# Kernel optimization log

Measured on AMD Instinct MI355X. Metric: run time of the kernel, lower is better.

## Reference

```python
import jax, jax.numpy as jnp
import numpy as np


def _bilinear_sample(image, flow):
    # image: [B,H,W,C] float32; flow: [B,H,W,2] float32
    B, H, W, C = image.shape
    h_f = jnp.float32(H)
    w_f = jnp.float32(W)

    # base grid in [-1, 1] via linspace (matches _linspace: step=(stop-start)/(num-1))
    xs = jnp.linspace(-1.0, 1.0, W, dtype=jnp.float32)  # [W]
    ys = jnp.linspace(-1.0, 1.0, H, dtype=jnp.float32)  # [H]
    x_base = jnp.broadcast_to(xs[None, None, :], (B, H, W)).reshape(-1)
    y_base = jnp.broadcast_to(ys[None, :, None], (B, H, W)).reshape(-1)

    flow_flat = flow.reshape(-1, 2)
    x = 0.3 * flow_flat[:, 0] + x_base  # [B*H*W]
    y = 0.3 * flow_flat[:, 1] + y_base

    # map to pixel coords; note original uses W/2 and H/2 (not (W-1)/2)
    x = (x + 1.0) * w_f / 2.0
    y = (y + 1.0) * h_f / 2.0

    x0 = jnp.floor(x).astype(jnp.int32)
    x1 = x0 + 1
    y0 = jnp.floor(y).astype(jnp.int32)
    y1 = y0 + 1
    x0 = jnp.clip(x0, 0, W - 1)
    x1 = jnp.clip(x1, 0, W - 1)
    y0 = jnp.clip(y0, 0, H - 1)
    y1 = jnp.clip(y1, 0, H - 1)

    base = jnp.repeat(jnp.arange(B, dtype=jnp.int32) * (H * W), H * W)  # [B*H*W]
    base_y0 = base + y0 * W
    base_y1 = base + y1 * W
    idx_a = base_y0 + x0
    idx_b = base_y1 + x0
    idx_c = base_y0 + x1
    idx_d = base_y1 + x1

    im_flat = image.reshape(-1, C)  # [B*H*W, C]
    Ia = im_flat[idx_a]
    Ib = im_flat[idx_b]
    Ic = im_flat[idx_c]
    Id = im_flat[idx_d]

    x0f = x0.astype(jnp.float32)
    x1f = x1.astype(jnp.float32)
    y0f = y0.astype(jnp.float32)
    y1f = y1.astype(jnp.float32)
    wa = ((x1f - x) * (y1f - y))[:, None]
    wb = ((x1f - x) * (y - y0f))[:, None]
    wc = ((x - x0f) * (y1f - y))[:, None]
    wd = ((x - x0f) * (y - y0f))[:, None]

    out = wa * Ia + wb * Ib + wc * Ic + wd * Id  # [B*H*W, C]
    return out.reshape(B, H, W, C)


def setup_inputs() -> dict:
    key = jax.random.key(0)
    k1, k2 = jax.random.split(key)
    image = jax.random.normal(k1, (16, 256, 256, 32), dtype=jnp.float32)
    flow = jax.random.normal(k2, (16, 256, 256, 2), dtype=jnp.float32)
    return {"image": image, "flow": flow}


def reference(image, flow):
    return _bilinear_sample(image, flow)
```

## Files before the change

### kernel.cpp

```cpp
#include <hip/hip_runtime.h>


__global__ __launch_bounds__(256) void bilinear_sampler_kernel(
    const float* __restrict__ image,
    const float* __restrict__ flow,
    float* __restrict__ out)
{
    constexpr int H = 256, W = 256, C = 32;

    const int gid = blockIdx.x * 256 + threadIdx.x;
    const int pid = gid >> 3;
    const int cq  = (gid & 7) << 2;

    const int b   = pid >> 16;
    const int rem = pid & 65535;
    const int yi  = rem >> 8;
    const int xi  = rem & 255;

    const float2 f = *reinterpret_cast<const float2*>(flow + (size_t)pid * 2);

    const float x_base = fmaf((float)xi, 2.0f / 255.0f, -1.0f);
    const float y_base = fmaf((float)yi, 2.0f / 255.0f, -1.0f);

    float x = fmaf(0.3f, f.x, x_base);
    float y = fmaf(0.3f, f.y, y_base);
    x = (x + 1.0f) * (0.5f * (float)W);
    y = (y + 1.0f) * (0.5f * (float)H);

    const float fx0 = floorf(x);
    const float fy0 = floorf(y);
    int x0 = (int)fx0;
    int y0 = (int)fy0;
    int x1 = x0 + 1;
    int y1 = y0 + 1;
    x0 = min(max(x0, 0), W - 1);
    x1 = min(max(x1, 0), W - 1);
    y0 = min(max(y0, 0), H - 1);
    y1 = min(max(y1, 0), H - 1);

    const float x0f = (float)x0, x1f = (float)x1;
    const float y0f = (float)y0, y1f = (float)y1;
    const float wa = (x1f - x) * (y1f - y);
    const float wb = (x1f - x) * (y - y0f);
    const float wc = (x - x0f) * (y1f - y);
    const float wd = (x - x0f) * (y - y0f);

    const int base = b << 16;
    const size_t row0 = (size_t)(base + y0 * W) * C;
    const size_t row1 = (size_t)(base + y1 * W) * C;

    const float4 Ia = *reinterpret_cast<const float4*>(image + row0 + (size_t)x0 * C + cq);
    const float4 Ib = *reinterpret_cast<const float4*>(image + row1 + (size_t)x0 * C + cq);
    const float4 Ic = *reinterpret_cast<const float4*>(image + row0 + (size_t)x1 * C + cq);
    const float4 Id = *reinterpret_cast<const float4*>(image + row1 + (size_t)x1 * C + cq);

    float4 o;
    o.x = wa * Ia.x + wb * Ib.x + wc * Ic.x + wd * Id.x;
    o.y = wa * Ia.y + wb * Ib.y + wc * Ic.y + wd * Id.y;
    o.z = wa * Ia.z + wb * Ib.z + wc * Ic.z + wd * Id.z;
    o.w = wa * Ia.w + wb * Ib.w + wc * Ic.w + wd * Id.w;

    *reinterpret_cast<float4*>(out + (size_t)pid * C + cq) = o;
}

extern "C" void kernel_launch(void* const* d_in, const int* in_sizes, int n_in,
                              void* d_out, int out_size, void* d_ws, size_t ws_size,
                              hipStream_t stream) {
    const float* image = (const float*)d_in[0];
    const float* flow  = (const float*)d_in[1];
    float* out = (float*)d_out;

    const int blocks = 8388608 / 256;
    bilinear_sampler_kernel<<<blocks, 256, 0, stream>>>(image, flow, out);
}
```

Before: 242.4 us.

## Process four pixels per thread with batched gathers and nontemporal stores

Each thread now handles four pixels spaced a quarter of the image apart, and the grid shrinks to a quarter of its size. All address and weight computations come first, then all sixteen float4 gathers are issued together to raise memory-level parallelism. Outputs are written with nontemporal stores to keep streaming writes from evicting gathered image data from cache. The cost is higher register pressure, which may lower occupancy, and more spread-out access across the image per thread.

```diff
diff --git a/kernel.cpp b/kernel.cpp
--- a/kernel.cpp
+++ b/kernel.cpp
@@ -1,5 +1,7 @@
 #include <hip/hip_runtime.h>
 
+
+using f32x4 = __attribute__((ext_vector_type(4))) float;
 
 __global__ __launch_bounds__(256) void bilinear_sampler_kernel(
     const float* __restrict__ image,
@@ -7,60 +9,75 @@
     float* __restrict__ out)
 {
     constexpr int H = 256, W = 256, C = 32;
+    constexpr int NPIX = 16 * H * W;
+    constexpr int PPT = 4;
+    constexpr int PSTRIDE = NPIX / PPT;
 
-    const int gid = blockIdx.x * 256 + threadIdx.x;
-    const int pid = gid >> 3;
-    const int cq  = (gid & 7) << 2;
+    const int gid  = blockIdx.x * 256 + threadIdx.x;
+    const int pid0 = gid >> 3;
+    const int cq   = (gid & 7) << 2;
 
-    const int b   = pid >> 16;
-    const int rem = pid & 65535;
-    const int yi  = rem >> 8;
-    const int xi  = rem & 255;
+    float wa[PPT], wb[PPT], wc[PPT], wd[PPT];
+    size_t a_a[PPT], a_b[PPT], a_c[PPT], a_d[PPT];
 
-    const float2 f = *reinterpret_cast<const float2*>(flow + (size_t)pid * 2);
+#pragma unroll
+    for (int k = 0; k < PPT; ++k) {
+        const int pid = pid0 + k * PSTRIDE;
+        const int b   = pid >> 16;
+        const int rem = pid & 65535;
+        const int yi  = rem >> 8;
+        const int xi  = rem & 255;
 
-    const float x_base = fmaf((float)xi, 2.0f / 255.0f, -1.0f);
-    const float y_base = fmaf((float)yi, 2.0f / 255.0f, -1.0f);
+        const float2 f = *reinterpret_cast<const float2*>(flow + (size_t)pid * 2);
 
-    float x = fmaf(0.3f, f.x, x_base);
-    float y = fmaf(0.3f, f.y, y_base);
-    x = (x + 1.0f) * (0.5f * (float)W);
-    y = (y + 1.0f) * (0.5f * (float)H);
+        const float x_base = fmaf((float)xi, 2.0f / 255.0f, -1.0f);
+        const float y_base = fmaf((float)yi, 2.0f / 255.0f, -1.0f);
 
-    const float fx0 = floorf(x);
-    const float fy0 = floorf(y);
-    int x0 = (int)fx0;
-    int y0 = (int)fy0;
-    int x1 = x0 + 1;
-    int y1 = y0 + 1;
-    x0 = min(max(x0, 0), W - 1);
-    x1 = min(max(x1, 0), W - 1);
-    y0 = min(max(y0, 0), H - 1);
-    y1 = min(max(y1, 0), H - 1);
+        float x = fmaf(0.3f, f.x, x_base);
+        float y = fmaf(0.3f, f.y, y_base);
+        x = (x + 1.0f) * (0.5f * (float)W);
+        y = (y + 1.0f) * (0.5f * (float)H);
 
-    const float x0f = (float)x0, x1f = (float)x1;
-    const float y0f = (float)y0, y1f = (float)y1;
-    const float wa = (x1f - x) * (y1f - y);
-    const float wb = (x1f - x) * (y - y0f);
-    const float wc = (x - x0f) * (y1f - y);
-    const float wd = (x - x0f) * (y - y0f);
+        int x0 = (int)floorf(x);
+        int y0 = (int)floorf(y);
+        int x1 = x0 + 1;
+        int y1 = y0 + 1;
+        x0 = min(max(x0, 0), W - 1);
+        x1 = min(max(x1, 0), W - 1);
+        y0 = min(max(y0, 0), H - 1);
+        y1 = min(max(y1, 0), H - 1);
 
-    const int base = b << 16;
-    const size_t row0 = (size_t)(base + y0 * W) * C;
-    const size_t row1 = (size_t)(base + y1 * W) * C;
+        const float x0f = (float)x0, x1f = (float)x1;
+        const float y0f = (float)y0, y1f = (float)y1;
+        wa[k] = (x1f - x) * (y1f - y);
+        wb[k] = (x1f - x) * (y - y0f);
+        wc[k] = (x - x0f) * (y1f - y);
+        wd[k] = (x - x0f) * (y - y0f);
 
-    const float4 Ia = *reinterpret_cast<const float4*>(image + row0 + (size_t)x0 * C + cq);
-    const float4 Ib = *reinterpret_cast<const float4*>(image + row1 + (size_t)x0 * C + cq);
-    const float4 Ic = *reinterpret_cast<const float4*>(image + row0 + (size_t)x1 * C + cq);
-    const float4 Id = *reinterpret_cast<const float4*>(image + row1 + (size_t)x1 * C + cq);
+        const int base = b << 16;
+        const size_t row0 = (size_t)(base + y0 * W) * C;
+        const size_t row1 = (size_t)(base + y1 * W) * C;
+        a_a[k] = row0 + (size_t)x0 * C + cq;
+        a_b[k] = row1 + (size_t)x0 * C + cq;
+        a_c[k] = row0 + (size_t)x1 * C + cq;
+        a_d[k] = row1 + (size_t)x1 * C + cq;
+    }
 
-    float4 o;
-    o.x = wa * Ia.x + wb * Ib.x + wc * Ic.x + wd * Id.x;
-    o.y = wa * Ia.y + wb * Ib.y + wc * Ic.y + wd * Id.y;
-    o.z = wa * Ia.z + wb * Ib.z + wc * Ic.z + wd * Id.z;
-    o.w = wa * Ia.w + wb * Ib.w + wc * Ic.w + wd * Id.w;
+    f32x4 Ia[PPT], Ib[PPT], Ic[PPT], Id[PPT];
+#pragma unroll
+    for (int k = 0; k < PPT; ++k) {
+        Ia[k] = *reinterpret_cast<const f32x4*>(image + a_a[k]);
+        Ib[k] = *reinterpret_cast<const f32x4*>(image + a_b[k]);
+        Ic[k] = *reinterpret_cast<const f32x4*>(image + a_c[k]);
+        Id[k] = *reinterpret_cast<const f32x4*>(image + a_d[k]);
+    }
 
-    *reinterpret_cast<float4*>(out + (size_t)pid * C + cq) = o;
+#pragma unroll
+    for (int k = 0; k < PPT; ++k) {
+        const int pid = pid0 + k * PSTRIDE;
+        f32x4 o = wa[k] * Ia[k] + wb[k] * Ib[k] + wc[k] * Ic[k] + wd[k] * Id[k];
+        __builtin_nontemporal_store(o, reinterpret_cast<f32x4*>(out + (size_t)pid * C + cq));
+    }
 }
 
 extern "C" void kernel_launch(void* const* d_in, const int* in_sizes, int n_in,
@@ -70,6 +87,6 @@
     const float* flow  = (const float*)d_in[1];
     float* out = (float*)d_out;
 
-    const int blocks = 8388608 / 256;
+    const int blocks = 2097152 / 256;
     bilinear_sampler_kernel<<<blocks, 256, 0, stream>>>(image, flow, out);
 }
```

Result: slower. 250.4 us (+3.3%).
